# Performance work log

Measured on AMD Instinct MI355X. Metric: run time of the kernel, lower is better.

The kernel has to match this reference:

```python
import jax, jax.numpy as jnp
import numpy as np

IN_Q = 256   # in_features // 4
OUT_Q = 256  # out_features // 4


def setup_inputs() -> dict:
    key = jax.random.key(0)
    kx, kr, ki, kj, kk = jax.random.split(key, 5)
    stdv = 1.0 / np.sqrt(IN_Q)
    return {
        "x": jax.random.normal(kx, (4, 8192, IN_Q * 4), dtype=jnp.float32),
        "r_weight": jax.random.uniform(kr, (OUT_Q, IN_Q), minval=-stdv, maxval=stdv, dtype=jnp.float32),
        "i_weight": jax.random.uniform(ki, (OUT_Q, IN_Q), minval=-stdv, maxval=stdv, dtype=jnp.float32),
        "j_weight": jax.random.uniform(kj, (OUT_Q, IN_Q), minval=-stdv, maxval=stdv, dtype=jnp.float32),
        "k_weight": jax.random.uniform(kk, (OUT_Q, IN_Q), minval=-stdv, maxval=stdv, dtype=jnp.float32),
        "bias": jnp.zeros((OUT_Q * 4,), dtype=jnp.float32),
    }


def reference(x, r_weight, i_weight, j_weight, k_weight, bias):
    batch_dims = x.shape[:-1]
    xq = x.reshape(*batch_dims, IN_Q, 4)  # [..., in_q, 4]
    r_x, i_x, j_x, k_x = xq[..., 0], xq[..., 1], xq[..., 2], xq[..., 3]

    lin = lambda v, w: jnp.einsum('...i,oi->...o', v, w)  # F.linear, no bias

    out_r = lin(r_x, r_weight) - lin(i_x, i_weight) - lin(j_x, j_weight) - lin(k_x, k_weight)
    out_i = lin(r_x, i_weight) + lin(i_x, r_weight) + lin(j_x, k_weight) - lin(k_x, j_weight)
    out_j = lin(r_x, j_weight) - lin(i_x, k_weight) + lin(j_x, r_weight) + lin(k_x, i_weight)
    out_k = lin(r_x, k_weight) + lin(i_x, j_weight) - lin(j_x, i_weight) + lin(k_x, r_weight)

    out = jnp.stack([out_r, out_i, out_j, out_k], axis=-1)  # [..., out_q, 4]
    out = out.reshape(*batch_dims, OUT_Q * 4)
    return out + bias
```

## Files before the change

### kernel.cpp

```cpp
#include <hip/hip_runtime.h>


typedef __attribute__((ext_vector_type(8))) short bf16x8;
typedef __attribute__((ext_vector_type(4))) float f32x4;

#define M_TOT 32768
#define N_TOT 1024
#define K_TOT 1024
#define BM 256
#define BN 256
#define BK 64
#define NKT (K_TOT / BK)

__device__ __forceinline__ unsigned short f2bf(float f) {
    union { float f; unsigned int u; } v; v.f = f;
    unsigned int u = v.u;
    u += 0x7fffu + ((u >> 16) & 1u);
    return (unsigned short)(u >> 16);
}

__device__ __forceinline__ bf16x8 cvt8(float4 a, float4 b) {
    bf16x8 r;
    r[0] = (short)f2bf(a.x); r[1] = (short)f2bf(a.y);
    r[2] = (short)f2bf(a.z); r[3] = (short)f2bf(a.w);
    r[4] = (short)f2bf(b.x); r[5] = (short)f2bf(b.y);
    r[6] = (short)f2bf(b.z); r[7] = (short)f2bf(b.w);
    return r;
}

__global__ __launch_bounds__(256) void build_w(const float* __restrict__ R,
                                               const float* __restrict__ I,
                                               const float* __restrict__ J,
                                               const float* __restrict__ Kw,
                                               ushort4* __restrict__ Wb) {
    int n = blockIdx.x;
    int i = threadIdx.x;
    int o = n >> 2, co = n & 3;
    int base = o * 256 + i;
    float r = R[base], ii = I[base], j = J[base], k = Kw[base];
    float v0, v1, v2, v3;
    if (co == 0)      { v0 = r;  v1 = -ii; v2 = -j;  v3 = -k; }
    else if (co == 1) { v0 = ii; v1 = r;   v2 = k;   v3 = -j; }
    else if (co == 2) { v0 = j;  v1 = -k;  v2 = r;   v3 = ii; }
    else              { v0 = k;  v1 = j;   v2 = -ii; v3 = r;  }
    ushort4 w;
    w.x = f2bf(v0); w.y = f2bf(v1); w.z = f2bf(v2); w.w = f2bf(v3);
    Wb[n * 256 + i] = w;
}

__device__ __forceinline__ void async_lds16(const void* g, void* l) {
    __builtin_amdgcn_global_load_lds(
        (const __attribute__((address_space(1))) unsigned int*)g,
        (__attribute__((address_space(3))) unsigned int*)l,
        16, 0, 0);
}

__device__ __forceinline__ void stage_ht(const unsigned short* __restrict__ G,
                                         int row0, int k0,
                                         unsigned short* ht,
                                         int wave, int lane) {
    int sr = lane >> 2;
    int sc = ((lane & 3) * 8) ^ ((lane & 32) ? 16 : 0);
#pragma unroll
    for (int j = 0; j < 2; ++j) {
        int si = j * 8 + wave;
        int rg = si >> 1, cg = si & 1;
        async_lds16(G + (size_t)(row0 + rg * 16 + sr) * K_TOT + k0 + cg * 32 + sc,
                    ht + si * 512);
    }
}

__global__ __launch_bounds__(512, 2) void gemm_fused(
        const float* __restrict__ X,
        const unsigned short* __restrict__ B,
        const float* __restrict__ bias,
        float* __restrict__ C) {
    __shared__ unsigned short smemA[2][2][8192];
    __shared__ unsigned short smemB[2][2][8192];

    const int tid  = threadIdx.x;
    const int wave = tid >> 6;
    const int lane = tid & 63;
    const int quad = lane >> 4;
    const int r16  = lane & 15;
    const int wm   = wave & 1;
    const int wn   = wave >> 1;

    int bid = blockIdx.x;
    int wg  = (bid & 7) * 64 + (bid >> 3);
    const int m0 = (wg >> 2) * BM;
    const int n0 = (wg & 3) * BN;

    const int laneRd = (r16 * 32 + quad * 8) ^ ((r16 & 8) << 1);
    const unsigned short* baseA = &smemA[0][wm][0] + laneRd;
    const unsigned short* baseB = &smemB[0][wn >> 1][0] + (wn & 1) * 4096 + laneRd;

    const int qrow = tid >> 2;
    const int ah   = qrow >> 6;
    const int r64  = qrow & 63;
    const int kb   = (tid & 3) * 16;
    const int wTerm = ah * 8192 +
        (((r64 >> 4) * 2 + (kb >> 5)) * 512 +
         ((((r64 & 15) * 32) + (kb & 31)) ^ ((r64 & 8) << 1)));
    unsigned short* baseW = &smemA[0][0][0] + wTerm;
    const float* gA = X + (size_t)(m0 + ah * 128 + r64) * K_TOT + kb;

    f32x4 acc[8][4];
#pragma unroll
    for (int i = 0; i < 8; ++i)
#pragma unroll
        for (int j = 0; j < 4; ++j)
            acc[i][j] = (f32x4){0.f, 0.f, 0.f, 0.f};

    float4 aq0, aq1, aq2, aq3;
    float4 bq0, bq1, bq2, bq3;

    {
        float4 p0 = *(const float4*)(gA + 0);
        float4 p1 = *(const float4*)(gA + 4);
        float4 p2 = *(const float4*)(gA + 8);
        float4 p3 = *(const float4*)(gA + 12);
        float4 q0 = *(const float4*)(gA + 65536 + 0);
        float4 q1 = *(const float4*)(gA + 65536 + 4);
        float4 q2 = *(const float4*)(gA + 65536 + 8);
        float4 q3 = *(const float4*)(gA + 65536 + 12);
        stage_ht(B, n0,       0, &smemB[0][0][0], wave, lane);
        stage_ht(B, n0 + 128, 0, &smemB[0][1][0], wave, lane);
        *(bf16x8*)(baseW + 0)        = cvt8(p0, p1);
        *(bf16x8*)(baseW + 8)        = cvt8(p2, p3);
        *(bf16x8*)(baseW + 4096)     = cvt8(q0, q1);
        *(bf16x8*)(baseW + 4096 + 8) = cvt8(q2, q3);
        p0 = *(const float4*)(gA + BK + 0);
        p1 = *(const float4*)(gA + BK + 4);
        p2 = *(const float4*)(gA + BK + 8);
        p3 = *(const float4*)(gA + BK + 12);
        q0 = *(const float4*)(gA + 65536 + BK + 0);
        q1 = *(const float4*)(gA + 65536 + BK + 4);
        q2 = *(const float4*)(gA + 65536 + BK + 8);
        q3 = *(const float4*)(gA + 65536 + BK + 12);
        *(bf16x8*)(baseW + 16384)        = cvt8(p0, p1);
        *(bf16x8*)(baseW + 16384 + 8)    = cvt8(p2, p3);
        *(bf16x8*)(baseW + 20480)        = cvt8(q0, q1);
        *(bf16x8*)(baseW + 20480 + 8)    = cvt8(q2, q3);
        aq0 = *(const float4*)(gA + 2 * BK + 0);
        aq1 = *(const float4*)(gA + 2 * BK + 4);
        aq2 = *(const float4*)(gA + 2 * BK + 8);
        aq3 = *(const float4*)(gA + 2 * BK + 12);
        asm volatile("s_waitcnt vmcnt(4)" ::: "memory");
        asm volatile("s_waitcnt lgkmcnt(0)" ::: "memory");
        __builtin_amdgcn_s_barrier();
    }

    bf16x8 af[4][2], bl[2][2], bh[2][2];

#pragma unroll 2
    for (int t = 0; t < NKT; ++t) {
        const int c  = t & 1;
        const int cA = c * 16384;

#pragma unroll
        for (int mb = 0; mb < 4; ++mb) {
            af[mb][0] = *(const bf16x8*)(baseA + cA + (mb * 2 + 0) * 512);
            af[mb][1] = *(const bf16x8*)(baseA + cA + (mb * 2 + 1) * 512);
        }
#pragma unroll
        for (int nb = 0; nb < 2; ++nb) {
            bl[nb][0] = *(const bf16x8*)(baseB + cA + (nb * 2 + 0) * 512);
            bl[nb][1] = *(const bf16x8*)(baseB + cA + (nb * 2 + 1) * 512);
        }
        if (t + 1 < NKT) {
            stage_ht(B, n0,       (t + 1) * BK, &smemB[c ^ 1][0][0], wave, lane);
            stage_ht(B, n0 + 128, (t + 1) * BK, &smemB[c ^ 1][1][0], wave, lane);
        }
        __builtin_amdgcn_s_barrier();
        asm volatile("s_waitcnt lgkmcnt(0)" ::: "memory");
        __builtin_amdgcn_s_setprio(1);
#pragma unroll
        for (int mb = 0; mb < 4; ++mb)
#pragma unroll
            for (int nb = 0; nb < 2; ++nb) {
                acc[mb][nb] = __builtin_amdgcn_mfma_f32_16x16x32_bf16(
                    af[mb][0], bl[nb][0], acc[mb][nb], 0, 0, 0);
                acc[mb][nb] = __builtin_amdgcn_mfma_f32_16x16x32_bf16(
                    af[mb][1], bl[nb][1], acc[mb][nb], 0, 0, 0);
            }
        __builtin_amdgcn_s_setprio(0);
        __builtin_amdgcn_s_barrier();

#pragma unroll
        for (int nb = 0; nb < 2; ++nb) {
            bh[nb][0] = *(const bf16x8*)(baseB + cA + ((nb + 2) * 2 + 0) * 512);
            bh[nb][1] = *(const bf16x8*)(baseB + cA + ((nb + 2) * 2 + 1) * 512);
        }
        if (t + 2 < NKT) {
            const int k2 = (t + 2) * BK;
            *(bf16x8*)(baseW + cA + 0) = cvt8(aq0, aq1);
            *(bf16x8*)(baseW + cA + 8) = cvt8(aq2, aq3);
            bq0 = *(const float4*)(gA + 65536 + k2 + 0);
            bq1 = *(const float4*)(gA + 65536 + k2 + 4);
            bq2 = *(const float4*)(gA + 65536 + k2 + 8);
            bq3 = *(const float4*)(gA + 65536 + k2 + 12);
        }
        __builtin_amdgcn_s_barrier();
        asm volatile("s_waitcnt lgkmcnt(0)" ::: "memory");
        __builtin_amdgcn_s_setprio(1);
#pragma unroll
        for (int mb = 0; mb < 4; ++mb)
#pragma unroll
            for (int nb = 0; nb < 2; ++nb) {
                acc[mb][nb + 2] = __builtin_amdgcn_mfma_f32_16x16x32_bf16(
                    af[mb][0], bh[nb][0], acc[mb][nb + 2], 0, 0, 0);
                acc[mb][nb + 2] = __builtin_amdgcn_mfma_f32_16x16x32_bf16(
                    af[mb][1], bh[nb][1], acc[mb][nb + 2], 0, 0, 0);
            }
        __builtin_amdgcn_s_setprio(0);
        __builtin_amdgcn_s_barrier();

#pragma unroll
        for (int mb = 0; mb < 4; ++mb) {
            af[mb][0] = *(const bf16x8*)(baseA + cA + ((mb + 4) * 2 + 0) * 512);
            af[mb][1] = *(const bf16x8*)(baseA + cA + ((mb + 4) * 2 + 1) * 512);
        }
        if (t + 3 < NKT) {
            const int k3 = (t + 3) * BK;
            aq0 = *(const float4*)(gA + k3 + 0);
            aq1 = *(const float4*)(gA + k3 + 4);
            aq2 = *(const float4*)(gA + k3 + 8);
            aq3 = *(const float4*)(gA + k3 + 12);
        }
        __builtin_amdgcn_s_barrier();
        asm volatile("s_waitcnt lgkmcnt(0)" ::: "memory");
        __builtin_amdgcn_s_setprio(1);
#pragma unroll
        for (int mb = 0; mb < 4; ++mb)
#pragma unroll
            for (int nb = 0; nb < 2; ++nb) {
                acc[mb + 4][nb + 2] = __builtin_amdgcn_mfma_f32_16x16x32_bf16(
                    af[mb][0], bh[nb][0], acc[mb + 4][nb + 2], 0, 0, 0);
                acc[mb + 4][nb + 2] = __builtin_amdgcn_mfma_f32_16x16x32_bf16(
                    af[mb][1], bh[nb][1], acc[mb + 4][nb + 2], 0, 0, 0);
            }
        __builtin_amdgcn_s_setprio(0);
        __builtin_amdgcn_s_barrier();

        __builtin_amdgcn_s_setprio(1);
#pragma unroll
        for (int mb = 0; mb < 4; ++mb)
#pragma unroll
            for (int nb = 0; nb < 2; ++nb) {
                acc[mb + 4][nb] = __builtin_amdgcn_mfma_f32_16x16x32_bf16(
                    af[mb][0], bl[nb][0], acc[mb + 4][nb], 0, 0, 0);
                acc[mb + 4][nb] = __builtin_amdgcn_mfma_f32_16x16x32_bf16(
                    af[mb][1], bl[nb][1], acc[mb + 4][nb], 0, 0, 0);
            }
        __builtin_amdgcn_s_setprio(0);
        if (t + 2 < NKT) {
            *(bf16x8*)(baseW + cA + 4096)     = cvt8(bq0, bq1);
            *(bf16x8*)(baseW + cA + 4096 + 8) = cvt8(bq2, bq3);
            asm volatile("s_waitcnt vmcnt(4)" ::: "memory");
        } else if (t + 1 < NKT) {
            asm volatile("s_waitcnt vmcnt(0)" ::: "memory");
        }
        asm volatile("s_waitcnt lgkmcnt(0)" ::: "memory");
        __builtin_amdgcn_s_barrier();
    }

    const int mbase = m0 + wm * 128 + quad * 4;
    const int nbase = n0 + wn * 64 + r16;
#pragma unroll
    for (int nb = 0; nb < 4; ++nb) {
        int col  = nbase + nb * 16;
        float bv = bias[col];
#pragma unroll
        for (int mb = 0; mb < 8; ++mb) {
            int rowb = mbase + mb * 16;
            f32x4 v  = acc[mb][nb];
#pragma unroll
            for (int r = 0; r < 4; ++r)
                C[(size_t)(rowb + r) * N_TOT + col] = v[r] + bv;
        }
    }
}

extern "C" void kernel_launch(void* const* d_in, const int* in_sizes, int n_in,
                              void* d_out, int out_size, void* d_ws, size_t ws_size,
                              hipStream_t stream) {
    const float* x    = (const float*)d_in[0];
    const float* rw   = (const float*)d_in[1];
    const float* iw   = (const float*)d_in[2];
    const float* jw   = (const float*)d_in[3];
    const float* kw   = (const float*)d_in[4];
    const float* bias = (const float*)d_in[5];
    float* out = (float*)d_out;

    unsigned short* Wb = (unsigned short*)d_ws;

    build_w<<<N_TOT, 256, 0, stream>>>(rw, iw, jw, kw, (ushort4*)Wb);

    gemm_fused<<<dim3((M_TOT / BM) * (N_TOT / BN)), 512, 0, stream>>>(
        x, Wb, bias, out);
}
```

Before: 315.3 us.

## Switch GEMM inner loop to 32x32x16 bf16 MFMA with new LDS staging layout

Replaces the 16x16x32 MFMA tiles with 32x32x16 bf16 MFMA. Each wave now holds a 4x2 grid of 32x32 accumulators, and the LDS read offsets, the swizzle, and the fp32-to-bf16 staging write pattern for X are reworked to match. This cuts the number of MFMA instructions and LDS fragment reads per tile, which should raise matrix-core throughput. The cost is more complex indexing, with a risk of LDS bank conflicts or layout mismatch errors in the new swizzle.

After: 296.5 us. 6.0% less time.

```diff
diff --git a/kernel.cpp b/kernel.cpp
--- a/kernel.cpp
+++ b/kernel.cpp
@@ -2,7 +2,7 @@
 
 
 typedef __attribute__((ext_vector_type(8))) short bf16x8;
-typedef __attribute__((ext_vector_type(4))) float f32x4;
+typedef __attribute__((ext_vector_type(16))) float f32x16;
 
 #define M_TOT 32768
 #define N_TOT 1024
@@ -81,8 +81,6 @@
     const int tid  = threadIdx.x;
     const int wave = tid >> 6;
     const int lane = tid & 63;
-    const int quad = lane >> 4;
-    const int r16  = lane & 15;
     const int wm   = wave & 1;
     const int wn   = wave >> 1;
 
@@ -91,67 +89,55 @@
     const int m0 = (wg >> 2) * BM;
     const int n0 = (wg & 3) * BN;
 
-    const int laneRd = (r16 * 32 + quad * 8) ^ ((r16 & 8) << 1);
+    const int laneRd = (lane & 15) * 32
+                     + ((lane >> 4) & 1) * 1024
+                     + ((lane >> 5) & 1) * 8;
+    const int kx  = (lane & 8) << 1;
+    const int kofs[2] = { kx, kx ^ 16 };
     const unsigned short* baseA = &smemA[0][wm][0] + laneRd;
     const unsigned short* baseB = &smemB[0][wn >> 1][0] + (wn & 1) * 4096 + laneRd;
 
-    const int qrow = tid >> 2;
-    const int ah   = qrow >> 6;
-    const int r64  = qrow & 63;
-    const int kb   = (tid & 3) * 16;
-    const int wTerm = ah * 8192 +
-        (((r64 >> 4) * 2 + (kb >> 5)) * 512 +
-         ((((r64 & 15) * 32) + (kb & 31)) ^ ((r64 & 8) << 1)));
-    unsigned short* baseW = &smemA[0][0][0] + wTerm;
-    const float* gA = X + (size_t)(m0 + ah * 128 + r64) * K_TOT + kb;
-
-    f32x4 acc[8][4];
-#pragma unroll
-    for (int i = 0; i < 8; ++i)
-#pragma unroll
-        for (int j = 0; j < 4; ++j)
-            acc[i][j] = (f32x4){0.f, 0.f, 0.f, 0.f};
-
-    float4 aq0, aq1, aq2, aq3;
-    float4 bq0, bq1, bq2, bq3;
-
-    {
-        float4 p0 = *(const float4*)(gA + 0);
-        float4 p1 = *(const float4*)(gA + 4);
-        float4 p2 = *(const float4*)(gA + 8);
-        float4 p3 = *(const float4*)(gA + 12);
-        float4 q0 = *(const float4*)(gA + 65536 + 0);
-        float4 q1 = *(const float4*)(gA + 65536 + 4);
-        float4 q2 = *(const float4*)(gA + 65536 + 8);
-        float4 q3 = *(const float4*)(gA + 65536 + 12);
-        stage_ht(B, n0,       0, &smemB[0][0][0], wave, lane);
-        stage_ht(B, n0 + 128, 0, &smemB[0][1][0], wave, lane);
-        *(bf16x8*)(baseW + 0)        = cvt8(p0, p1);
-        *(bf16x8*)(baseW + 8)        = cvt8(p2, p3);
-        *(bf16x8*)(baseW + 4096)     = cvt8(q0, q1);
-        *(bf16x8*)(baseW + 4096 + 8) = cvt8(q2, q3);
-        p0 = *(const float4*)(gA + BK + 0);
-        p1 = *(const float4*)(gA + BK + 4);
-        p2 = *(const float4*)(gA + BK + 8);
-        p3 = *(const float4*)(gA + BK + 12);
-        q0 = *(const float4*)(gA + 65536 + BK + 0);
-        q1 = *(const float4*)(gA + 65536 + BK + 4);
-        q2 = *(const float4*)(gA + 65536 + BK + 8);
-        q3 = *(const float4*)(gA + 65536 + BK + 12);
-        *(bf16x8*)(baseW + 16384)        = cvt8(p0, p1);
-        *(bf16x8*)(baseW + 16384 + 8)    = cvt8(p2, p3);
-        *(bf16x8*)(baseW + 20480)        = cvt8(q0, q1);
-        *(bf16x8*)(baseW + 20480 + 8)    = cvt8(q2, q3);
-        aq0 = *(const float4*)(gA + 2 * BK + 0);
-        aq1 = *(const float4*)(gA + 2 * BK + 4);
-        aq2 = *(const float4*)(gA + 2 * BK + 8);
-        aq3 = *(const float4*)(gA + 2 * BK + 12);
-        asm volatile("s_waitcnt vmcnt(4)" ::: "memory");
-        asm volatile("s_waitcnt lgkmcnt(0)" ::: "memory");
-        __builtin_amdgcn_s_barrier();
-    }
-
-    bf16x8 af[4][2], bl[2][2], bh[2][2];
+    const int srow = (lane >> 2) & 15;
+    const int skc  = lane & 3;
+    unsigned short* wbase = &smemA[0][0][0] + wave * 512
+                          + (((srow * 32) + skc * 8) ^ ((lane & 32) ? 16 : 0));
+    const float* gBase = X + (size_t)(m0 + (wave >> 1) * 16 + srow) * K_TOT
+                       + (wave & 1) * 32 + skc * 8;
+
+    f32x16 acc[4][2];
+#pragma unroll
+    for (int i = 0; i < 4; ++i)
+#pragma unroll
+        for (int j = 0; j < 2; ++j)
+#pragma unroll
+            for (int r = 0; r < 16; ++r)
+                acc[i][j][r] = 0.f;
+
+    float4 aq0a, aq0b, aq1a, aq1b;
+    float4 bq0a, bq0b, bq1a, bq1b;
+
+    stage_ht(B, n0,       0, &smemB[0][0][0], wave, lane);
+    stage_ht(B, n0 + 128, 0, &smemB[0][1][0], wave, lane);
+#pragma unroll
+    for (int tt = 0; tt < 2; ++tt)
+#pragma unroll
+        for (int rh = 0; rh < 2; ++rh)
+#pragma unroll
+            for (int h = 0; h < 2; ++h) {
+                const float* g = gBase + (size_t)h * 131072 + rh * 65536 + tt * BK;
+                float4 a = *(const float4*)g;
+                float4 b = *(const float4*)(g + 4);
+                *(bf16x8*)(wbase + tt * 16384 + h * 8192 + rh * 4096) = cvt8(a, b);
+            }
+    aq0a = *(const float4*)(gBase + 2 * BK);
+    aq0b = *(const float4*)(gBase + 2 * BK + 4);
+    aq1a = *(const float4*)(gBase + 131072 + 2 * BK);
+    aq1b = *(const float4*)(gBase + 131072 + 2 * BK + 4);
+    asm volatile("s_waitcnt vmcnt(4)" ::: "memory");
+    asm volatile("s_waitcnt lgkmcnt(0)" ::: "memory");
+    __builtin_amdgcn_s_barrier();
+
+    bf16x8 af[2][4], bl[4], bh[4];
 
 #pragma unroll 2
     for (int t = 0; t < NKT; ++t) {
@@ -159,15 +145,14 @@
         const int cA = c * 16384;
 
 #pragma unroll
-        for (int mb = 0; mb < 4; ++mb) {
-            af[mb][0] = *(const bf16x8*)(baseA + cA + (mb * 2 + 0) * 512);
-            af[mb][1] = *(const bf16x8*)(baseA + cA + (mb * 2 + 1) * 512);
-        }
-#pragma unroll
-        for (int nb = 0; nb < 2; ++nb) {
-            bl[nb][0] = *(const bf16x8*)(baseB + cA + (nb * 2 + 0) * 512);
-            bl[nb][1] = *(const bf16x8*)(baseB + cA + (nb * 2 + 1) * 512);
-        }
+        for (int rb = 0; rb < 2; ++rb)
+#pragma unroll
+            for (int ks = 0; ks < 4; ++ks)
+                af[rb][ks] = *(const bf16x8*)(baseA + cA + rb * 2048
+                                              + (ks >> 1) * 512 + kofs[ks & 1]);
+#pragma unroll
+        for (int ks = 0; ks < 4; ++ks)
+            bl[ks] = *(const bf16x8*)(baseB + cA + (ks >> 1) * 512 + kofs[ks & 1]);
         if (t + 1 < NKT) {
             stage_ht(B, n0,       (t + 1) * BK, &smemB[c ^ 1][0][0], wave, lane);
             stage_ht(B, n0 + 128, (t + 1) * BK, &smemB[c ^ 1][1][0], wave, lane);
@@ -176,87 +161,75 @@
         asm volatile("s_waitcnt lgkmcnt(0)" ::: "memory");
         __builtin_amdgcn_s_setprio(1);
 #pragma unroll
-        for (int mb = 0; mb < 4; ++mb)
-#pragma unroll
-            for (int nb = 0; nb < 2; ++nb) {
-                acc[mb][nb] = __builtin_amdgcn_mfma_f32_16x16x32_bf16(
-                    af[mb][0], bl[nb][0], acc[mb][nb], 0, 0, 0);
-                acc[mb][nb] = __builtin_amdgcn_mfma_f32_16x16x32_bf16(
-                    af[mb][1], bl[nb][1], acc[mb][nb], 0, 0, 0);
-            }
-        __builtin_amdgcn_s_setprio(0);
-        __builtin_amdgcn_s_barrier();
-
-#pragma unroll
-        for (int nb = 0; nb < 2; ++nb) {
-            bh[nb][0] = *(const bf16x8*)(baseB + cA + ((nb + 2) * 2 + 0) * 512);
-            bh[nb][1] = *(const bf16x8*)(baseB + cA + ((nb + 2) * 2 + 1) * 512);
-        }
+        for (int rb = 0; rb < 2; ++rb)
+#pragma unroll
+            for (int ks = 0; ks < 4; ++ks)
+                acc[rb][0] = __builtin_amdgcn_mfma_f32_32x32x16_bf16(
+                    af[rb][ks], bl[ks], acc[rb][0], 0, 0, 0);
+        __builtin_amdgcn_s_setprio(0);
+        __builtin_amdgcn_s_barrier();
+
+#pragma unroll
+        for (int ks = 0; ks < 4; ++ks)
+            bh[ks] = *(const bf16x8*)(baseB + cA + 2048
+                                      + (ks >> 1) * 512 + kofs[ks & 1]);
         if (t + 2 < NKT) {
             const int k2 = (t + 2) * BK;
-            *(bf16x8*)(baseW + cA + 0) = cvt8(aq0, aq1);
-            *(bf16x8*)(baseW + cA + 8) = cvt8(aq2, aq3);
-            bq0 = *(const float4*)(gA + 65536 + k2 + 0);
-            bq1 = *(const float4*)(gA + 65536 + k2 + 4);
-            bq2 = *(const float4*)(gA + 65536 + k2 + 8);
-            bq3 = *(const float4*)(gA + 65536 + k2 + 12);
-        }
-        __builtin_amdgcn_s_barrier();
-        asm volatile("s_waitcnt lgkmcnt(0)" ::: "memory");
-        __builtin_amdgcn_s_setprio(1);
-#pragma unroll
-        for (int mb = 0; mb < 4; ++mb)
-#pragma unroll
-            for (int nb = 0; nb < 2; ++nb) {
-                acc[mb][nb + 2] = __builtin_amdgcn_mfma_f32_16x16x32_bf16(
-                    af[mb][0], bh[nb][0], acc[mb][nb + 2], 0, 0, 0);
-                acc[mb][nb + 2] = __builtin_amdgcn_mfma_f32_16x16x32_bf16(
-                    af[mb][1], bh[nb][1], acc[mb][nb + 2], 0, 0, 0);
-            }
-        __builtin_amdgcn_s_setprio(0);
-        __builtin_amdgcn_s_barrier();
-
-#pragma unroll
-        for (int mb = 0; mb < 4; ++mb) {
-            af[mb][0] = *(const bf16x8*)(baseA + cA + ((mb + 4) * 2 + 0) * 512);
-            af[mb][1] = *(const bf16x8*)(baseA + cA + ((mb + 4) * 2 + 1) * 512);
-        }
+            *(bf16x8*)(wbase + cA)        = cvt8(aq0a, aq0b);
+            *(bf16x8*)(wbase + cA + 8192) = cvt8(aq1a, aq1b);
+            bq0a = *(const float4*)(gBase + 65536 + k2);
+            bq0b = *(const float4*)(gBase + 65536 + k2 + 4);
+            bq1a = *(const float4*)(gBase + 131072 + 65536 + k2);
+            bq1b = *(const float4*)(gBase + 131072 + 65536 + k2 + 4);
+        }
+        __builtin_amdgcn_s_barrier();
+        asm volatile("s_waitcnt lgkmcnt(0)" ::: "memory");
+        __builtin_amdgcn_s_setprio(1);
+#pragma unroll
+        for (int rb = 0; rb < 2; ++rb)
+#pragma unroll
+            for (int ks = 0; ks < 4; ++ks)
+                acc[rb][1] = __builtin_amdgcn_mfma_f32_32x32x16_bf16(
+                    af[rb][ks], bh[ks], acc[rb][1], 0, 0, 0);
+        __builtin_amdgcn_s_setprio(0);
+        __builtin_amdgcn_s_barrier();
+
+#pragma unroll
+        for (int rb = 0; rb < 2; ++rb)
+#pragma unroll
+            for (int ks = 0; ks < 4; ++ks)
+                af[rb][ks] = *(const bf16x8*)(baseA + cA + (rb + 2) * 2048
+                                              + (ks >> 1) * 512 + kofs[ks & 1]);
         if (t + 3 < NKT) {
             const int k3 = (t + 3) * BK;
-            aq0 = *(const float4*)(gA + k3 + 0);
-            aq1 = *(const float4*)(gA + k3 + 4);
-            aq2 = *(const float4*)(gA + k3 + 8);
-            aq3 = *(const float4*)(gA + k3 + 12);
-        }
-        __builtin_amdgcn_s_barrier();
-        asm volatile("s_waitcnt lgkmcnt(0)" ::: "memory");
-        __builtin_amdgcn_s_setprio(1);
-#pragma unroll
-        for (int mb = 0; mb < 4; ++mb)
-#pragma unroll
-            for (int nb = 0; nb < 2; ++nb) {
-                acc[mb + 4][nb + 2] = __builtin_amdgcn_mfma_f32_16x16x32_bf16(
-                    af[mb][0], bh[nb][0], acc[mb + 4][nb + 2], 0, 0, 0);
-                acc[mb + 4][nb + 2] = __builtin_amdgcn_mfma_f32_16x16x32_bf16(
-                    af[mb][1], bh[nb][1], acc[mb + 4][nb + 2], 0, 0, 0);
-            }
-        __builtin_amdgcn_s_setprio(0);
-        __builtin_amdgcn_s_barrier();
-
-        __builtin_amdgcn_s_setprio(1);
-#pragma unroll
-        for (int mb = 0; mb < 4; ++mb)
-#pragma unroll
-            for (int nb = 0; nb < 2; ++nb) {
-                acc[mb + 4][nb] = __builtin_amdgcn_mfma_f32_16x16x32_bf16(
-                    af[mb][0], bl[nb][0], acc[mb + 4][nb], 0, 0, 0);
-                acc[mb + 4][nb] = __builtin_amdgcn_mfma_f32_16x16x32_bf16(
-                    af[mb][1], bl[nb][1], acc[mb + 4][nb], 0, 0, 0);
-            }
+            aq0a = *(const float4*)(gBase + k3);
+            aq0b = *(const float4*)(gBase + k3 + 4);
+            aq1a = *(const float4*)(gBase + 131072 + k3);
+            aq1b = *(const float4*)(gBase + 131072 + k3 + 4);
+        }
+        __builtin_amdgcn_s_barrier();
+        asm volatile("s_waitcnt lgkmcnt(0)" ::: "memory");
+        __builtin_amdgcn_s_setprio(1);
+#pragma unroll
+        for (int rb = 0; rb < 2; ++rb)
+#pragma unroll
+            for (int ks = 0; ks < 4; ++ks)
+                acc[rb + 2][1] = __builtin_amdgcn_mfma_f32_32x32x16_bf16(
+                    af[rb][ks], bh[ks], acc[rb + 2][1], 0, 0, 0);
+        __builtin_amdgcn_s_setprio(0);
+        __builtin_amdgcn_s_barrier();
+
+        __builtin_amdgcn_s_setprio(1);
+#pragma unroll
+        for (int rb = 0; rb < 2; ++rb)
+#pragma unroll
+            for (int ks = 0; ks < 4; ++ks)
+                acc[rb + 2][0] = __builtin_amdgcn_mfma_f32_32x32x16_bf16(
+                    af[rb][ks], bl[ks], acc[rb + 2][0], 0, 0, 0);
         __builtin_amdgcn_s_setprio(0);
         if (t + 2 < NKT) {
-            *(bf16x8*)(baseW + cA + 4096)     = cvt8(bq0, bq1);
-            *(bf16x8*)(baseW + cA + 4096 + 8) = cvt8(bq2, bq3);
+            *(bf16x8*)(wbase + cA + 4096)        = cvt8(bq0a, bq0b);
+            *(bf16x8*)(wbase + cA + 8192 + 4096) = cvt8(bq1a, bq1b);
             asm volatile("s_waitcnt vmcnt(4)" ::: "memory");
         } else if (t + 1 < NKT) {
             asm volatile("s_waitcnt vmcnt(0)" ::: "memory");
@@ -265,19 +238,20 @@
         __builtin_amdgcn_s_barrier();
     }
 
-    const int mbase = m0 + wm * 128 + quad * 4;
-    const int nbase = n0 + wn * 64 + r16;
-#pragma unroll
-    for (int nb = 0; nb < 4; ++nb) {
-        int col  = nbase + nb * 16;
+    const int mbase = m0 + wm * 128 + ((lane >> 5) & 1) * 4;
+    const int nbase = n0 + wn * 64 + (lane & 31);
+#pragma unroll
+    for (int cb = 0; cb < 2; ++cb) {
+        int col  = nbase + cb * 32;
         float bv = bias[col];
 #pragma unroll
-        for (int mb = 0; mb < 8; ++mb) {
-            int rowb = mbase + mb * 16;
-            f32x4 v  = acc[mb][nb];
-#pragma unroll
-            for (int r = 0; r < 4; ++r)
-                C[(size_t)(rowb + r) * N_TOT + col] = v[r] + bv;
+        for (int rb = 0; rb < 4; ++rb) {
+            f32x16 v = acc[rb][cb];
+#pragma unroll
+            for (int r = 0; r < 16; ++r) {
+                int row = mbase + rb * 32 + (r & 3) + (r >> 2) * 8;
+                C[(size_t)row * N_TOT + col] = v[r] + bv;
+            }
         }
     }
 }
```
